# Kernel optimization log

Hardware: AMD Instinct MI355X
Metric: run time of the kernel (lower is better)

## Reference

```python
import jax, jax.numpy as jnp
import numpy as np

B, S, D, L, H = 2, 2048, 2048, 3, 16
DH = D // H
BLOCK = 16
NA = 64
Q = NA * BLOCK
KV = S + Q
VOCAB = 32000
MASK_ID = 31999
GAMMA = 7.0
EPS = 1e-6


def _rope(x, pos):
    # x: [B,H,T,DH], pos: [B,T]
    half = DH // 2
    inv = 1.0 / (10000.0 ** (jnp.arange(half, dtype=jnp.float32) / half))
    ang = pos[:, None, :, None].astype(jnp.float32) * inv  # [B,1,T,half]
    c, s = jnp.cos(ang), jnp.sin(ang)
    x1, x2 = x[..., :half], x[..., half:]
    return jnp.concatenate([x1 * c - x2 * s, x2 * c + x1 * s], axis=-1)


def setup_inputs() -> dict:
    key = jax.random.key(0)
    ks = jax.random.split(key, 12)
    w = lambda k, shp: 0.02 * jax.random.normal(k, shp, jnp.float32)
    return {
        'input_ids': jax.random.randint(ks[0], (B, S), 0, VOCAB, dtype=jnp.int32),
        'hidden_states': jax.random.normal(ks[1], (L, B, S, D), jnp.float32),
        'loss_mask': jnp.ones((B, S), jnp.int32),
        'lm_head_weight': w(ks[2], (VOCAB, D)),
        'norm_weight': jnp.ones((D,), jnp.float32),
        'anchor_positions': jnp.sort(jax.random.randint(ks[3], (B, NA), 0, S - BLOCK, dtype=jnp.int32), axis=-1),
        'ctx_proj_w': w(ks[4], (D, L * D)),
        'embed_table': w(ks[5], (VOCAB, D)),
        'wq': w(ks[6], (D, D)),
        'wk': w(ks[7], (D, D)),
        'wv': w(ks[8], (D, D)),
        'wo': w(ks[9], (D, D)),
    }


def reference(input_ids, hidden_states, loss_mask, lm_head_weight, norm_weight,
              anchor_positions, ctx_proj_w, embed_table, wq, wk, wv, wo):
    # --- context feature: concat L target-layer hiddens, project to D ---
    ctx_cat = jnp.transpose(hidden_states, (1, 2, 0, 3)).reshape(B, S, L * D)
    ctx = jnp.einsum('bsf,df->bsd', ctx_cat, ctx_proj_w)

    # --- position ids (context: 0..S-1; draft block i starts at anchor_i) ---
    ctx_pos = jnp.broadcast_to(jnp.arange(S, dtype=jnp.int32), (B, S))
    draft_pos = (anchor_positions[:, :, None] + jnp.arange(BLOCK, dtype=jnp.int32)[None, None, :]).reshape(B, Q)

    # --- draft input (anchor token + MASKs) and labels ---
    off = jnp.arange(Q, dtype=jnp.int32) % BLOCK                       # [Q]
    anchor_per_tok = jnp.repeat(anchor_positions, BLOCK, axis=1)       # [B,Q]
    anchor_tok = jnp.take_along_axis(input_ids, anchor_positions, axis=1)
    draft_ids = jnp.where(off[None, :] == 0, jnp.repeat(anchor_tok, BLOCK, axis=1), MASK_ID)
    labels = jnp.where(off[None, :] == 0, -100,
                       jnp.take_along_axis(input_ids, anchor_per_tok + off[None, :], axis=1))

    # --- block-causal mask: [B,Q,KV] ---
    qi = jnp.arange(Q, dtype=jnp.int32)
    ki = jnp.arange(KV, dtype=jnp.int32)
    qb = qi // BLOCK                                                   # [Q]
    apos = anchor_positions[:, qb]                                     # [B,Q]
    ctx_vis = (ki[None, None, :] < S) & (ki[None, None, :] < apos[:, :, None])
    kb = (ki - S) // BLOCK
    draft_vis = (ki >= S)[None, :] & (qb[:, None] == kb[None, :])      # [Q,KV]
    mask = ctx_vis | draft_vis[None]                                   # [B,Q,KV]

    # --- single RoPE attention layer: draft queries over [context; draft] ---
    emb = embed_table[draft_ids]                                       # [B,Q,D]
    x_kv = jnp.concatenate([ctx, emb], axis=1)                         # [B,KV,D]
    pos_kv = jnp.concatenate([ctx_pos, draft_pos], axis=1)             # [B,KV]
    q = _rope((emb @ wq.T).reshape(B, Q, H, DH).transpose(0, 2, 1, 3), draft_pos)
    k = _rope((x_kv @ wk.T).reshape(B, KV, H, DH).transpose(0, 2, 1, 3), pos_kv)
    v = (x_kv @ wv.T).reshape(B, KV, H, DH).transpose(0, 2, 1, 3)
    scores = jnp.einsum('bhqd,bhkd->bhqk', q, k) / np.float32(np.sqrt(DH))
    scores = jnp.where(mask[:, None], scores, jnp.float32(-1e30))
    attn = jax.nn.softmax(scores, axis=-1)
    out = jnp.einsum('bhqk,bhkd->bhqd', attn, v).transpose(0, 2, 1, 3).reshape(B, Q, D) @ wo.T
    hidden = emb + out

    # --- RMSNorm + LM head ---
    hidden = hidden * jax.lax.rsqrt(jnp.mean(hidden * hidden, -1, keepdims=True) + EPS) * norm_weight
    logits = hidden @ lm_head_weight.T                                 # [B,Q,VOCAB]

    # --- decay-weighted CE loss + accuracy ---
    logp = jax.nn.log_softmax(logits, axis=-1)
    lab = jnp.where(labels < 0, 0, labels)
    nll = -jnp.take_along_axis(logp, lab[..., None], axis=-1)[..., 0]
    valid = labels != -100
    offf = off.astype(jnp.float32)
    decay = jnp.where(off == 0, 0.0, jnp.exp(-(offf - 1.0) / GAMMA))   # [Q]
    w = decay[None, :] * valid.astype(jnp.float32)
    loss = jnp.sum(nll * w) / jnp.maximum(jnp.sum(w), 1e-6)
    preds = jnp.argmax(logits, axis=-1).astype(labels.dtype)
    acc = jnp.sum((preds == labels) & valid) / jnp.maximum(jnp.sum(valid), 1)
    return loss, acc.astype(jnp.float32)
```

## Files before the change

### kernel.cpp

```cpp
#include <hip/hip_runtime.h>

#define B_ 2
#define S_ 2048
#define D_ 2048
#define L_ 3
#define H_ 16
#define DH_ 128
#define BLK_ 16
#define NA_ 64
#define Q_ 1024
#define KV_ 3072
#define VOCAB_ 32000
#define MASK_ID_ 31999
#define NTOK_ (B_*Q_)
#define VT2_ (VOCAB_/256)
#define NCHUNK_ 4

typedef __attribute__((ext_vector_type(8))) short bf16x8;
typedef __attribute__((ext_vector_type(4))) float f32x4;
typedef const __attribute__((address_space(1))) void* gptr_t;
typedef __attribute__((address_space(3))) void* lptr_t;

__device__ inline unsigned short f2bf(float x) {
  unsigned int u = __float_as_uint(x);
  unsigned int r = (u + 0x7fff + ((u >> 16) & 1)) >> 16;
  return (unsigned short)r;
}
__device__ inline float bf2f(unsigned short u) {
  return __uint_as_float(((unsigned int)u) << 16);
}

__global__ void k_meta(const int* __restrict__ ids, const int* __restrict__ anchors,
                       int* __restrict__ dids, int* __restrict__ dpos, int* __restrict__ labels) {
  int t = blockIdx.x * 256 + threadIdx.x;
  if (t >= NTOK_) return;
  int b = t >> 10, qi = t & 1023;
  int a = qi >> 4, off = qi & 15;
  int ap = anchors[b * NA_ + a];
  dpos[t] = ap + off;
  dids[t] = (off == 0) ? ids[b * S_ + ap] : MASK_ID_;
  labels[t] = (off == 0) ? -100 : ids[b * S_ + ap + off];
}

__global__ void k_cvt(const float* __restrict__ in, unsigned short* __restrict__ out, int n4) {
  int i = blockIdx.x * 256 + threadIdx.x;
  if (i >= n4) return;
  float4 v = ((const float4*)in)[i];
  ushort4 o;
  o.x = f2bf(v.x); o.y = f2bf(v.y); o.z = f2bf(v.z); o.w = f2bf(v.w);
  ((ushort4*)out)[i] = o;
}

__global__ void k_cvt_ctx(const float* __restrict__ hs, unsigned short* __restrict__ out) {
  int bi = blockIdx.x;
  int l = bi % 3, row = bi / 3;
  const float4* src = (const float4*)(hs + ((size_t)l * B_ * S_ + row) * (size_t)D_);
  ushort4* dst = (ushort4*)(out + (size_t)row * (3 * D_) + (size_t)l * D_);
  for (int i = threadIdx.x; i < D_ / 4; i += 256) {
    float4 v = src[i];
    ushort4 o;
    o.x = f2bf(v.x); o.y = f2bf(v.y); o.z = f2bf(v.z); o.w = f2bf(v.w);
    dst[i] = o;
  }
}

__global__ void k_gather(const float* __restrict__ table, const int* __restrict__ dids,
                         unsigned short* __restrict__ x_kv) {
  int row = blockIdx.x;
  int b = row >> 10, qi = row & 1023;
  const float4* src = (const float4*)(table + (size_t)dids[row] * D_);
  ushort4* dst = (ushort4*)(x_kv + ((size_t)b * KV_ + S_ + qi) * D_);
  for (int i = threadIdx.x; i < D_ / 4; i += 256) {
    float4 v = src[i];
    ushort4 o;
    o.x = f2bf(v.x); o.y = f2bf(v.y); o.z = f2bf(v.z); o.w = f2bf(v.w);
    dst[i] = o;
  }
}

#define STAGE2(buf_, kt_)                                                      \
  {                                                                            \
    _Pragma("unroll")                                                          \
    for (int i_ = 0; i_ < 4; ++i_) {                                           \
      __builtin_amdgcn_global_load_lds((gptr_t)(A + aoff[i_] + (kt_)),         \
          (lptr_t)((char*)Asl2 + (buf_) * 32768 + abase[i_]), 16, 0, 0);       \
      __builtin_amdgcn_global_load_lds((gptr_t)(Bw + boff[i_] + (kt_)),        \
          (lptr_t)((char*)Bsl2 + (buf_) * 32768 + bbase[i_]), 16, 0, 0);       \
    }                                                                          \
  }

__global__ __launch_bounds__(512, 1) void k_gemm2(
    const unsigned short* __restrict__ A, const unsigned short* __restrict__ Bw,
    int M, int N, int K,
    const int* __restrict__ labels, float* __restrict__ pm, float* __restrict__ ps,
    int* __restrict__ pbi, float* __restrict__ plab) {
  __shared__ unsigned short Asl2[2 * 256 * 64];
  __shared__ unsigned short Bsl2[2 * 256 * 64];
  int ntm = M >> 8;
  int per = gridDim.x >> 3;
  int wgid = (blockIdx.x & 7) * per + (blockIdx.x >> 3);
  int by = wgid % ntm, bx = wgid / ntm;
  int rowbase = by << 8, colbase = bx << 8;
  int tid = threadIdx.x, l = tid & 63, w = tid >> 6;
  int wm = w >> 2, wn = w & 3;
  int lo = l & 15, hi = l >> 4;

  long long aoff[4], boff[4];
  int abase[4], bbase[4];
#pragma unroll
  for (int i = 0; i < 4; ++i) {
    int rb8 = (w * 4 + i) * 8;
    int r = rb8 + (l >> 3);
    int cu = (l & 7) ^ (r & 7);
    aoff[i] = (long long)(rowbase + r) * K + cu * 8;
    boff[i] = (long long)(colbase + r) * K + cu * 8;
    abase[i] = rb8 * 128;
    bbase[i] = rb8 * 128;
  }
  int ard[8][2], brd[4][2];
#pragma unroll
  for (int m = 0; m < 8; ++m)
#pragma unroll
    for (int ks = 0; ks < 2; ++ks) {
      int r = wm * 128 + m * 16 + lo;
      int p = ((ks << 2) | hi) ^ (r & 7);
      ard[m][ks] = r * 64 + p * 8;
    }
#pragma unroll
  for (int n = 0; n < 4; ++n)
#pragma unroll
    for (int ks = 0; ks < 2; ++ks) {
      int r = wn * 64 + n * 16 + lo;
      int p = ((ks << 2) | hi) ^ (r & 7);
      brd[n][ks] = r * 64 + p * 8;
    }

  f32x4 acc[8][4];
#pragma unroll
  for (int m = 0; m < 8; ++m)
#pragma unroll
    for (int n = 0; n < 4; ++n) acc[m][n] = (f32x4){0.f, 0.f, 0.f, 0.f};

  int NT = K >> 6;
  int cur = 0;
  STAGE2(0, 0);
  for (int t = 0; t < NT; ++t) {
    if (t + 1 < NT) {
      STAGE2(cur ^ 1, (t + 1) << 6);
      asm volatile("s_waitcnt vmcnt(8)" ::: "memory");
    } else {
      asm volatile("s_waitcnt vmcnt(0)" ::: "memory");
    }
    __builtin_amdgcn_s_barrier();
    asm volatile("" ::: "memory");
    const unsigned short* as_ = Asl2 + cur * 16384;
    const unsigned short* bs_ = Bsl2 + cur * 16384;
    __builtin_amdgcn_s_setprio(1);
#pragma unroll
    for (int ks = 0; ks < 2; ++ks) {
      bf16x8 af[8], bg[4];
#pragma unroll
      for (int m = 0; m < 8; ++m) af[m] = *(const bf16x8*)(as_ + ard[m][ks]);
#pragma unroll
      for (int n = 0; n < 4; ++n) bg[n] = *(const bf16x8*)(bs_ + brd[n][ks]);
#pragma unroll
      for (int m = 0; m < 8; ++m)
#pragma unroll
        for (int n = 0; n < 4; ++n)
          acc[m][n] = __builtin_amdgcn_mfma_f32_16x16x32_bf16(af[m], bg[n], acc[m][n], 0, 0, 0);
    }
    __builtin_amdgcn_s_setprio(0);
    __builtin_amdgcn_sched_barrier(0);
    asm volatile("" ::: "memory");
    __builtin_amdgcn_s_barrier();
    cur ^= 1;
  }

  float* f = (float*)Asl2;
  int* ii = (int*)Bsl2;
  __syncthreads();
  if (tid < 256) { f[2304 + tid] = -3.0e38f; ii[1280 + tid] = labels[rowbase + tid]; }
  __syncthreads();
#pragma unroll
  for (int m = 0; m < 8; ++m)
#pragma unroll
    for (int r4 = 0; r4 < 4; ++r4) {
      int rl = wm * 128 + m * 16 + hi * 4 + r4;
      float mx = acc[m][0][r4];
      int arg = colbase + wn * 64 + lo;
#pragma unroll
      for (int n = 1; n < 4; ++n) {
        float v = acc[m][n][r4];
        int c = colbase + wn * 64 + n * 16 + lo;
        if (v > mx) { mx = v; arg = c; }
      }
#pragma unroll
      for (int d = 1; d < 16; d <<= 1) {
        float om = __shfl_xor(mx, d);
        int oc = __shfl_xor(arg, d);
        if (om > mx || (om == mx && oc < arg)) { mx = om; arg = oc; }
      }
      if (lo == 0) { f[wn * 256 + rl] = mx; ii[wn * 256 + rl] = arg; }
    }
  __syncthreads();
  if (tid < 256) {
    float m0 = f[tid]; int a0 = ii[tid];
#pragma unroll
    for (int x = 1; x < 4; ++x) {
      float v = f[x * 256 + tid]; int c = ii[x * 256 + tid];
      if (v > m0 || (v == m0 && c < a0)) { m0 = v; a0 = c; }
    }
    f[2048 + tid] = m0; ii[1024 + tid] = a0;
  }
  __syncthreads();
#pragma unroll
  for (int m = 0; m < 8; ++m)
#pragma unroll
    for (int r4 = 0; r4 < 4; ++r4) {
      int rl = wm * 128 + m * 16 + hi * 4 + r4;
      float gm = f[2048 + rl];
      float sacc = 0.f;
#pragma unroll
      for (int n = 0; n < 4; ++n) sacc += __expf(acc[m][n][r4] - gm);
#pragma unroll
      for (int d = 1; d < 16; d <<= 1) sacc += __shfl_xor(sacc, d);
      if (lo == 0) f[1024 + wn * 256 + rl] = sacc;
      int lab = ii[1280 + rl];
      int rel = lab - colbase;
      if (rel >= 0 && rel < 256 && (rel >> 6) == wn && (rel & 15) == lo) {
        int n_own = (rel >> 4) & 3;
#pragma unroll
        for (int n = 0; n < 4; ++n)
          if (n == n_own) f[2304 + rl] = acc[m][n][r4];
      }
    }
  __syncthreads();
  if (tid < 256) {
    int grow = rowbase + tid;
    size_t p = (size_t)grow * VT2_ + bx;
    pm[p] = f[2048 + tid];
    ps[p] = f[1024 + tid] + f[1024 + 256 + tid] + f[1024 + 512 + tid] + f[1024 + 768 + tid];
    pbi[p] = ii[1024 + tid];
    plab[p] = f[2304 + tid];
  }
}

template <int CMODE>
__global__ __launch_bounds__(256) void k_mfma_bt(
    const unsigned short* __restrict__ A, const unsigned short* __restrict__ Bw,
    float* __restrict__ Cf, unsigned short* __restrict__ Cb,
    int M, int N, int K, int adivlog, long long abump, int cdivlog, long long cbump) {
  __shared__ unsigned short As[128 * 32];
  __shared__ unsigned short Bs[128 * 32];
  int ntn = N >> 7;
  int bx = blockIdx.x % ntn, by = blockIdx.x / ntn;
  int rowbase = by << 7, colbase = bx << 7;
  int tid = threadIdx.x, lane = tid & 63, w = tid >> 6;
  int wr = w >> 1, wc = w & 1;
  int lo = lane & 15, hi = lane >> 4;

  f32x4 acc[4][4];
#pragma unroll
  for (int m = 0; m < 4; ++m)
#pragma unroll
    for (int n = 0; n < 4; ++n) acc[m][n] = (f32x4){0.f, 0.f, 0.f, 0.f};

  for (int kt = 0; kt < K; kt += 32) {
#pragma unroll
    for (int i = 0; i < 2; ++i) {
      int seg = i * 4 + w;
      int rloc = seg * 16 + (lane >> 2);
      int kcol = kt + ((lane & 3) << 3);
      int ra = rowbase + rloc;
      long long aoff = (long long)ra * K + (long long)(ra >> adivlog) * abump + kcol;
      __builtin_amdgcn_global_load_lds((gptr_t)(A + aoff), (lptr_t)(As + seg * 512), 16, 0, 0);
      int rb = colbase + rloc;
      long long boff = (long long)rb * K + kcol;
      __builtin_amdgcn_global_load_lds((gptr_t)(Bw + boff), (lptr_t)(Bs + seg * 512), 16, 0, 0);
    }
    __syncthreads();
    bf16x8 af[4], bfv[4];
#pragma unroll
    for (int m = 0; m < 4; ++m) {
      int row = wr * 64 + m * 16 + lo;
      af[m] = *(const bf16x8*)(As + row * 32 + (hi << 3));
    }
#pragma unroll
    for (int n = 0; n < 4; ++n) {
      int row = wc * 64 + n * 16 + lo;
      bfv[n] = *(const bf16x8*)(Bs + row * 32 + (hi << 3));
    }
#pragma unroll
    for (int m = 0; m < 4; ++m)
#pragma unroll
      for (int n = 0; n < 4; ++n)
        acc[m][n] = __builtin_amdgcn_mfma_f32_16x16x32_bf16(af[m], bfv[n], acc[m][n], 0, 0, 0);
    __syncthreads();
  }

  if (CMODE == 0 || CMODE == 1) {
#pragma unroll
    for (int m = 0; m < 4; ++m)
#pragma unroll
      for (int n = 0; n < 4; ++n)
#pragma unroll
        for (int r4 = 0; r4 < 4; ++r4) {
          int row = rowbase + wr * 64 + m * 16 + hi * 4 + r4;
          int col = colbase + wc * 64 + n * 16 + lo;
          size_t addr = (size_t)row * N + (size_t)(row >> cdivlog) * cbump + col;
          if (CMODE == 0) Cf[addr] = acc[m][n][r4];
          else Cb[addr] = f2bf(acc[m][n][r4]);
        }
  } else {
#pragma unroll
    for (int m = 0; m < 4; ++m)
#pragma unroll
      for (int n = 0; n < 4; ++n)
#pragma unroll
        for (int r4 = 0; r4 < 4; ++r4) {
          int row = rowbase + wr * 64 + m * 16 + hi * 4 + r4;
          int col = colbase + wc * 64 + n * 16 + lo;
          int bb = row >= KV_;
          int kv = row - bb * KV_;
          size_t addr = ((size_t)(bb * H_ + (col >> 7)) * 128 + (col & 127)) * KV_ + kv;
          Cb[addr] = f2bf(acc[m][n][r4]);
        }
  }
}

__global__ void k_rope(unsigned short* __restrict__ x, const int* __restrict__ dpos, int mode) {
  int idx = blockIdx.x * 256 + threadIdx.x;
  int j = idx & 63;
  int h = (idx >> 6) & 15;
  int row = idx >> 10;
  int pos;
  if (mode == 0) {
    if (row >= NTOK_) return;
    pos = dpos[row];
  } else {
    if (row >= B_ * KV_) return;
    int b = row / KV_, kvi = row % KV_;
    pos = (kvi < S_) ? kvi : dpos[b * Q_ + (kvi - S_)];
  }
  float inv = expf(-(float)j * (9.210340371976184f / 64.f));
  float ang = (float)pos * inv;
  float c = cosf(ang), s = sinf(ang);
  unsigned short* p = x + (size_t)row * D_ + h * DH_ + j;
  float x1 = bf2f(p[0]), x2 = bf2f(p[64]);
  p[0] = f2bf(x1 * c - x2 * s);
  p[64] = f2bf(x2 * c + x1 * s);
}

__global__ __launch_bounds__(256) void k_attn_part(
    const unsigned short* __restrict__ qb, const unsigned short* __restrict__ kb,
    const unsigned short* __restrict__ vt, const int* __restrict__ anchors,
    float* __restrict__ pm_att, float* __restrict__ pl_att, float* __restrict__ po_att) {
  __shared__ __align__(16) unsigned short P_all[4][16 * 40];
  int w = threadIdx.x >> 6, lane = threadIdx.x & 63;
  int blk = blockIdx.x * 4 + w;
  int chunk = blk & 3, h = (blk >> 2) & 15, a = (blk >> 6) & 63, b = blk >> 12;
  int ql = lane & 15, p = lane >> 4;
  int apos = anchors[b * NA_ + a];

  int cstart = chunk << 9;
  int cend = min(apos, cstart + 512);
  int len = (cend > cstart) ? (cend - cstart) : 0;
  int ntile = (len + 31) >> 5;
  int total = ntile + ((chunk == 3) ? 1 : 0);

  if (total == 0) {
    if (p == 0) { pm_att[blk * 16 + ql] = -3.0e38f; pl_att[blk * 16 + ql] = 0.f; }
    return;
  }
  unsigned short* P = P_all[w];

  const unsigned short* qbase = qb + ((size_t)(b * Q_ + a * 16 + ql)) * D_ + h * DH_;
  bf16x8 qf[4];
#pragma unroll
  for (int ks = 0; ks < 4; ++ks)
    qf[ks] = *(const bf16x8*)(qbase + ks * 32 + p * 8);

  const unsigned short* kbb = kb + (size_t)b * KV_ * D_ + h * DH_;
  const unsigned short* vtb = vt + ((size_t)(b * H_ + h)) * 128 * KV_;

  f32x4 o[8];
#pragma unroll
  for (int nt = 0; nt < 8; ++nt) o[nt] = (f32x4){0.f, 0.f, 0.f, 0.f};
  float mrun = -3.0e38f, lrun = 0.f;
  const float scl = 0.08838834764831845f;

  for (int t = 0; t < total; ++t) {
    bool isdraft = (chunk == 3) && (t == ntile);
    int ktb = isdraft ? (S_ + a * 16) : (cstart + (t << 5));
    int vc = isdraft ? 16 : min(32, cend - ktb);
    float s[2][4];
#pragma unroll
    for (int g = 0; g < 2; ++g) {
      if (g * 16 < vc) {
        f32x4 accs = (f32x4){0.f, 0.f, 0.f, 0.f};
        const unsigned short* krow = kbb + (size_t)(ktb + g * 16 + ql) * D_;
#pragma unroll
        for (int ks = 0; ks < 4; ++ks) {
          bf16x8 kf = *(const bf16x8*)(krow + ks * 32 + p * 8);
          accs = __builtin_amdgcn_mfma_f32_16x16x32_bf16(kf, qf[ks], accs, 0, 0, 0);
        }
#pragma unroll
        for (int r = 0; r < 4; ++r) {
          int kl = g * 16 + p * 4 + r;
          s[g][r] = (kl < vc) ? accs[r] * scl : -3.0e38f;
        }
      } else {
#pragma unroll
        for (int r = 0; r < 4; ++r) s[g][r] = -3.0e38f;
      }
    }
    float mt = s[0][0];
#pragma unroll
    for (int g = 0; g < 2; ++g)
#pragma unroll
      for (int r = 0; r < 4; ++r) mt = fmaxf(mt, s[g][r]);
    mt = fmaxf(mt, __shfl_xor(mt, 16));
    mt = fmaxf(mt, __shfl_xor(mt, 32));
    float mnew = fmaxf(mrun, mt);
    float corr = __expf(mrun - mnew);
    float psum = 0.f;
#pragma unroll
    for (int g = 0; g < 2; ++g) {
      float p0 = __expf(s[g][0] - mnew), p1 = __expf(s[g][1] - mnew);
      float p2 = __expf(s[g][2] - mnew), p3 = __expf(s[g][3] - mnew);
      psum += p0 + p1 + p2 + p3;
      ushort2 w0, w1;
      w0.x = f2bf(p0); w0.y = f2bf(p1); w1.x = f2bf(p2); w1.y = f2bf(p3);
      int eo = ql * 40 + g * 16 + p * 4;
      *(ushort2*)(P + eo) = w0;
      *(ushort2*)(P + eo + 2) = w1;
    }
    psum += __shfl_xor(psum, 16);
    psum += __shfl_xor(psum, 32);
    lrun = lrun * corr + psum;
    mrun = mnew;
    float cr[4];
#pragma unroll
    for (int r = 0; r < 4; ++r) cr[r] = __shfl(corr, p * 4 + r);
#pragma unroll
    for (int nt = 0; nt < 8; ++nt)
#pragma unroll
      for (int r = 0; r < 4; ++r) o[nt][r] *= cr[r];
    bf16x8 pf = *(const bf16x8*)(P + ql * 40 + p * 8);
#pragma unroll
    for (int nt = 0; nt < 8; ++nt) {
      bf16x8 vf = *(const bf16x8*)(vtb + (size_t)(nt * 16 + ql) * KV_ + ktb + p * 8);
      o[nt] = __builtin_amdgcn_mfma_f32_16x16x32_bf16(pf, vf, o[nt], 0, 0, 0);
    }
  }
  if (p == 0) { pm_att[blk * 16 + ql] = mrun; pl_att[blk * 16 + ql] = lrun; }
  float* pob = po_att + (size_t)blk * 2048;
#pragma unroll
  for (int nt = 0; nt < 8; ++nt)
#pragma unroll
    for (int r = 0; r < 4; ++r)
      pob[(p * 4 + r) * 128 + nt * 16 + ql] = o[nt][r];
}

__global__ __launch_bounds__(256) void k_attn_combine(
    const float* __restrict__ pm_att, const float* __restrict__ pl_att,
    const float* __restrict__ po_att, unsigned short* __restrict__ ob) {
  int base = blockIdx.x;
  int h = base & 15, a = (base >> 4) & 63, b = base >> 10;
  int d = threadIdx.x & 127, qh = threadIdx.x >> 7;
  int pbase = base * 4;
#pragma unroll
  for (int qq = 0; qq < 8; ++qq) {
    int q = qh * 8 + qq;
    float m0 = pm_att[(pbase + 0) * 16 + q], m1 = pm_att[(pbase + 1) * 16 + q];
    float m2 = pm_att[(pbase + 2) * 16 + q], m3 = pm_att[(pbase + 3) * 16 + q];
    float mg = fmaxf(fmaxf(m0, m1), fmaxf(m2, m3));
    float w0 = __expf(m0 - mg), w1 = __expf(m1 - mg);
    float w2 = __expf(m2 - mg), w3 = __expf(m3 - mg);
    float lg = pl_att[(pbase + 0) * 16 + q] * w0 + pl_att[(pbase + 1) * 16 + q] * w1 +
               pl_att[(pbase + 2) * 16 + q] * w2 + pl_att[(pbase + 3) * 16 + q] * w3;
    float od = po_att[(size_t)(pbase + 0) * 2048 + q * 128 + d] * w0 +
               po_att[(size_t)(pbase + 1) * 2048 + q * 128 + d] * w1 +
               po_att[(size_t)(pbase + 2) * 2048 + q * 128 + d] * w2 +
               po_att[(size_t)(pbase + 3) * 2048 + q * 128 + d] * w3;
    ob[((size_t)(b * Q_ + a * 16 + q)) * D_ + h * DH_ + d] = f2bf(od / lg);
  }
}

__global__ void k_rmsnorm(const unsigned short* __restrict__ x_kv, const float* __restrict__ proj,
                          const float* __restrict__ nw, unsigned short* __restrict__ outp) {
  int row = blockIdx.x;
  int b = row >> 10, qi = row & 1023;
  const unsigned short* emb = x_kv + ((size_t)b * KV_ + S_ + qi) * D_;
  const float* pr = proj + (size_t)row * D_;
  __shared__ float red[256];
  float h[8];
  float ssum = 0.f;
#pragma unroll
  for (int i = 0; i < 8; ++i) {
    int d = threadIdx.x + i * 256;
    h[i] = bf2f(emb[d]) + pr[d];
    ssum += h[i] * h[i];
  }
  red[threadIdx.x] = ssum;
  __syncthreads();
  for (int s = 128; s; s >>= 1) {
    if (threadIdx.x < s) red[threadIdx.x] += red[threadIdx.x + s];
    __syncthreads();
  }
  float scale = rsqrtf(red[0] / (float)D_ + 1e-6f);
#pragma unroll
  for (int i = 0; i < 8; ++i) {
    int d = threadIdx.x + i * 256;
    outp[(size_t)row * D_ + d] = f2bf(h[i] * scale * nw[d]);
  }
}

__global__ void k_combine(const float* __restrict__ pm, const float* __restrict__ ps,
                          const int* __restrict__ pbi, const float* __restrict__ plab,
                          const int* __restrict__ labels, float* __restrict__ ts) {
  int t = blockIdx.x * 256 + threadIdx.x;
  if (t >= NTOK_) return;
  const float* pmr = pm + (size_t)t * VT2_;
  const float* psr = ps + (size_t)t * VT2_;
  const int* pbir = pbi + (size_t)t * VT2_;
  const float* plabr = plab + (size_t)t * VT2_;
  float M = -3.0e38f; int bi = 0;
  for (int x = 0; x < VT2_; ++x) {
    float v = pmr[x];
    if (v > M) { M = v; bi = pbir[x]; }
  }
  float ssum = 0.f, labl = -3.0e38f;
  for (int x = 0; x < VT2_; ++x) {
    ssum += psr[x] * __expf(pmr[x] - M);
    labl = fmaxf(labl, plabr[x]);
  }
  float lse = M + logf(ssum);
  int lab = labels[t];
  int off = t & 15;
  float valid = (lab != -100) ? 1.f : 0.f;
  float w = (off == 0) ? 0.f : __expf(-(float)(off - 1) / 7.0f);
  w *= valid;
  float nll = (lab != -100) ? (lse - labl) : 0.f;
  float correct = (valid > 0.f && bi == lab) ? 1.f : 0.f;
  ts[t * 4 + 0] = nll * w;
  ts[t * 4 + 1] = w;
  ts[t * 4 + 2] = correct;
  ts[t * 4 + 3] = valid;
}

__global__ void k_finalize(const float* __restrict__ ts, float* __restrict__ out) {
  __shared__ float r0[256], r1[256], r2[256], r3[256];
  int tid = threadIdx.x;
  float s0 = 0, s1 = 0, s2 = 0, s3 = 0;
  for (int t = tid; t < NTOK_; t += 256) {
    s0 += ts[t * 4 + 0]; s1 += ts[t * 4 + 1];
    s2 += ts[t * 4 + 2]; s3 += ts[t * 4 + 3];
  }
  r0[tid] = s0; r1[tid] = s1; r2[tid] = s2; r3[tid] = s3;
  __syncthreads();
  for (int s = 128; s; s >>= 1) {
    if (tid < s) {
      r0[tid] += r0[tid + s]; r1[tid] += r1[tid + s];
      r2[tid] += r2[tid + s]; r3[tid] += r3[tid + s];
    }
    __syncthreads();
  }
  if (tid == 0) {
    out[0] = r0[0] / fmaxf(r1[0], 1e-6f);
    out[1] = r2[0] / fmaxf(r3[0], 1.f);
  }
}

extern "C" void kernel_launch(void* const* d_in, const int* in_sizes, int n_in,
                              void* d_out, int out_size, void* d_ws, size_t ws_size,
                              hipStream_t stream) {
  const int* input_ids = (const int*)d_in[0];
  const float* hs = (const float*)d_in[1];
  const float* lm_head = (const float*)d_in[3];
  const float* norm_w = (const float*)d_in[4];
  const int* anchors = (const int*)d_in[5];
  const float* ctx_w = (const float*)d_in[6];
  const float* embed = (const float*)d_in[7];
  const float* wq = (const float*)d_in[8];
  const float* wk = (const float*)d_in[9];
  const float* wv = (const float*)d_in[10];
  const float* wo = (const float*)d_in[11];
  float* out = (float*)d_out;

  char* base = (char*)d_ws;
  size_t off = 0;
  unsigned short* x_kv_bf = (unsigned short*)(base + off); off += (size_t)B_ * KV_ * D_ * 2;
  unsigned short* wkb = (unsigned short*)(base + off); off += (size_t)D_ * D_ * 2;
  unsigned short* wvb = (unsigned short*)(base + off); off += (size_t)D_ * D_ * 2;
  unsigned short* wqb = (unsigned short*)(base + off); off += (size_t)D_ * D_ * 2;
  unsigned short* wob = (unsigned short*)(base + off); off += (size_t)D_ * D_ * 2;
  unsigned short* hidden_bf = (unsigned short*)(base + off); off += (size_t)NTOK_ * D_ * 2;
  unsigned short* attn_bf = (unsigned short*)(base + off); off += (size_t)NTOK_ * D_ * 2;
  float* proj = (float*)(base + off); off += (size_t)NTOK_ * D_ * 4;
  float* pm = (float*)(base + off); off += (size_t)NTOK_ * VT2_ * 4;
  float* psum = (float*)(base + off); off += (size_t)NTOK_ * VT2_ * 4;
  float* plab = (float*)(base + off); off += (size_t)NTOK_ * VT2_ * 4;
  int* pbi = (int*)(base + off); off += (size_t)NTOK_ * VT2_ * 4;
  float* tstats = (float*)(base + off); off += (size_t)NTOK_ * 4 * 4;
  int* dids = (int*)(base + off); off += NTOK_ * 4;
  int* dpos = (int*)(base + off); off += NTOK_ * 4;
  int* labels = (int*)(base + off); off += NTOK_ * 4;
  char* regA = base + off;
  const size_t SLACK = 65536;
  unsigned short* ctxA = (unsigned short*)(regA);
  unsigned short* ctx_wbf = (unsigned short*)(regA + 50331648);
  unsigned short* kbuf = (unsigned short*)(regA + 50331648 + 25165824);
  unsigned short* vtbuf = (unsigned short*)(regA + 50331648 + 2 * 25165824 + SLACK);
  unsigned short* qbuf = (unsigned short*)(regA + 50331648 + 3 * 25165824 + 2 * SLACK);
  unsigned short* lm_bf = (unsigned short*)(regA);
  float* po_att = (float*)(regA);
  float* pm_att = (float*)(regA + 67108864);
  float* pl_att = (float*)(regA + 67108864 + 524288);

  k_meta<<<(NTOK_ + 255) / 256, 256, 0, stream>>>(input_ids, anchors, dids, dpos, labels);
  k_cvt<<<((D_ * (L_ * D_) / 4) + 255) / 256, 256, 0, stream>>>(ctx_w, ctx_wbf, D_ * (L_ * D_) / 4);
  k_cvt<<<((D_ * D_ / 4) + 255) / 256, 256, 0, stream>>>(wk, wkb, D_ * D_ / 4);
  k_cvt<<<((D_ * D_ / 4) + 255) / 256, 256, 0, stream>>>(wv, wvb, D_ * D_ / 4);
  k_cvt<<<((D_ * D_ / 4) + 255) / 256, 256, 0, stream>>>(wq, wqb, D_ * D_ / 4);
  k_cvt<<<((D_ * D_ / 4) + 255) / 256, 256, 0, stream>>>(wo, wob, D_ * D_ / 4);
  k_cvt_ctx<<<B_ * S_ * L_, 256, 0, stream>>>(hs, ctxA);
  k_gather<<<NTOK_, 256, 0, stream>>>(embed, dids, x_kv_bf);

  k_mfma_bt<1><<<(4096 / 128) * (2048 / 128), 256, 0, stream>>>(
      ctxA, ctx_wbf, nullptr, x_kv_bf, 4096, 2048, 6144, 30, 0LL, 11, (long long)Q_ * D_);
  k_mfma_bt<1><<<(6144 / 128) * (2048 / 128), 256, 0, stream>>>(
      x_kv_bf, wkb, nullptr, kbuf, 6144, 2048, 2048, 30, 0LL, 30, 0LL);
  k_mfma_bt<3><<<(6144 / 128) * (2048 / 128), 256, 0, stream>>>(
      x_kv_bf, wvb, nullptr, vtbuf, 6144, 2048, 2048, 30, 0LL, 30, 0LL);
  k_mfma_bt<1><<<(2048 / 128) * (2048 / 128), 256, 0, stream>>>(
      x_kv_bf + (size_t)S_ * D_, wqb, nullptr, qbuf, 2048, 2048, 2048, 10,
      (long long)(KV_ - Q_) * D_, 30, 0LL);
  k_rope<<<(NTOK_ * H_ * 64) / 256, 256, 0, stream>>>(qbuf, dpos, 0);
  k_rope<<<(B_ * KV_ * H_ * 64) / 256, 256, 0, stream>>>(kbuf, dpos, 1);
  k_attn_part<<<(B_ * NA_ * H_ * NCHUNK_) / 4, 256, 0, stream>>>(
      qbuf, kbuf, vtbuf, anchors, pm_att, pl_att, po_att);
  k_attn_combine<<<B_ * NA_ * H_, 256, 0, stream>>>(pm_att, pl_att, po_att, attn_bf);
  k_mfma_bt<0><<<(2048 / 128) * (2048 / 128), 256, 0, stream>>>(
      attn_bf, wob, proj, nullptr, 2048, 2048, 2048, 30, 0LL, 30, 0LL);
  k_rmsnorm<<<NTOK_, 256, 0, stream>>>(x_kv_bf, proj, norm_w, hidden_bf);
  k_cvt<<<((VOCAB_ * D_ / 4) + 255) / 256, 256, 0, stream>>>(lm_head, lm_bf, VOCAB_ * D_ / 4);
  k_gemm2<<<(2048 / 256) * (VOCAB_ / 256), 512, 0, stream>>>(
      hidden_bf, lm_bf, 2048, VOCAB_, 2048, labels, pm, psum, pbi, plab);
  k_combine<<<(NTOK_ + 255) / 256, 256, 0, stream>>>(pm, psum, pbi, plab, labels, tstats);
  k_finalize<<<1, 256, 0, stream>>>(tstats, out);
}
```

Before: 1.211 ms.

## Add double-buffered 128x256 direct-to-LDS GEMM for context and K projections

Adds a new 512-thread GEMM kernel with 128x256 tiles and a K-step of 64. Tiles are loaded straight into LDS with global_load_lds, using XOR-swizzled layouts and two buffers so the next tile loads while the current one is computed. Blocks are remapped across XCD-sized groups to improve L2 locality. The kernel replaces the 128x128 generic GEMM for the context projection and the K projection, aiming for more reuse per tile and better overlap of memory and compute, at the cost of larger LDS use and one workgroup per CU.

```diff
diff --git a/kernel.cpp b/kernel.cpp
--- a/kernel.cpp
+++ b/kernel.cpp
@@ -243,6 +243,123 @@
     pbi[p] = ii[1024 + tid];
     plab[p] = f[2304 + tid];
   }
+}
+
+#define STAGE2B(buf_, kt_)                                                     \
+  {                                                                            \
+    _Pragma("unroll")                                                          \
+    for (int i_ = 0; i_ < 2; ++i_)                                             \
+      __builtin_amdgcn_global_load_lds((gptr_t)(A + aoff[i_] + (kt_)),         \
+          (lptr_t)((char*)Asl + (buf_) * 16384 + abase[i_]), 16, 0, 0);        \
+    _Pragma("unroll")                                                          \
+    for (int i_ = 0; i_ < 4; ++i_)                                             \
+      __builtin_amdgcn_global_load_lds((gptr_t)(Bw + boff[i_] + (kt_)),        \
+          (lptr_t)((char*)Bsl + (buf_) * 32768 + bbase[i_]), 16, 0, 0);        \
+  }
+
+__global__ __launch_bounds__(512, 1) void k_gemm2b(
+    const unsigned short* __restrict__ A, const unsigned short* __restrict__ Bw,
+    unsigned short* __restrict__ Cb,
+    int M, int N, int K, int cdivlog, long long cbump) {
+  __shared__ unsigned short Asl[2 * 128 * 64];
+  __shared__ unsigned short Bsl[2 * 256 * 64];
+  int ntm = M >> 7;
+  int per = gridDim.x >> 3;
+  int wgid = (blockIdx.x & 7) * per + (blockIdx.x >> 3);
+  int by = wgid % ntm, bx = wgid / ntm;
+  int rowbase = by << 7, colbase = bx << 8;
+  int tid = threadIdx.x, l = tid & 63, w = tid >> 6;
+  int wm = w >> 2, wn = w & 3;
+  int lo = l & 15, hi = l >> 4;
+
+  long long aoff[2]; int abase[2];
+#pragma unroll
+  for (int i = 0; i < 2; ++i) {
+    int rb8 = i * 64 + w * 8;
+    int r = rb8 + (l >> 3);
+    int cu = (l & 7) ^ (r & 7);
+    aoff[i] = (long long)(rowbase + r) * K + cu * 8;
+    abase[i] = rb8 * 128;
+  }
+  long long boff[4]; int bbase[4];
+#pragma unroll
+  for (int i = 0; i < 4; ++i) {
+    int rb8 = (w * 4 + i) * 8;
+    int r = rb8 + (l >> 3);
+    int cu = (l & 7) ^ (r & 7);
+    boff[i] = (long long)(colbase + r) * K + cu * 8;
+    bbase[i] = rb8 * 128;
+  }
+  int ard[4][2], brd[4][2];
+#pragma unroll
+  for (int m = 0; m < 4; ++m)
+#pragma unroll
+    for (int ks = 0; ks < 2; ++ks) {
+      int r = wm * 64 + m * 16 + lo;
+      int p = ((ks << 2) | hi) ^ (r & 7);
+      ard[m][ks] = r * 64 + p * 8;
+    }
+#pragma unroll
+  for (int n = 0; n < 4; ++n)
+#pragma unroll
+    for (int ks = 0; ks < 2; ++ks) {
+      int r = wn * 64 + n * 16 + lo;
+      int p = ((ks << 2) | hi) ^ (r & 7);
+      brd[n][ks] = r * 64 + p * 8;
+    }
+
+  f32x4 acc[4][4];
+#pragma unroll
+  for (int m = 0; m < 4; ++m)
+#pragma unroll
+    for (int n = 0; n < 4; ++n) acc[m][n] = (f32x4){0.f, 0.f, 0.f, 0.f};
+
+  int NT = K >> 6;
+  int cur = 0;
+  STAGE2B(0, 0);
+  for (int t = 0; t < NT; ++t) {
+    if (t + 1 < NT) {
+      STAGE2B(cur ^ 1, (t + 1) << 6);
+      asm volatile("s_waitcnt vmcnt(6)" ::: "memory");
+    } else {
+      asm volatile("s_waitcnt vmcnt(0)" ::: "memory");
+    }
+    __builtin_amdgcn_s_barrier();
+    asm volatile("" ::: "memory");
+    const unsigned short* as_ = Asl + cur * 8192;
+    const unsigned short* bs_ = Bsl + cur * 16384;
+    __builtin_amdgcn_s_setprio(1);
+#pragma unroll
+    for (int ks = 0; ks < 2; ++ks) {
+      bf16x8 af[4], bg[4];
+#pragma unroll
+      for (int m = 0; m < 4; ++m) af[m] = *(const bf16x8*)(as_ + ard[m][ks]);
+#pragma unroll
+      for (int n = 0; n < 4; ++n) bg[n] = *(const bf16x8*)(bs_ + brd[n][ks]);
+#pragma unroll
+      for (int m = 0; m < 4; ++m)
+#pragma unroll
+        for (int n = 0; n < 4; ++n)
+          acc[m][n] = __builtin_amdgcn_mfma_f32_16x16x32_bf16(af[m], bg[n], acc[m][n], 0, 0, 0);
+    }
+    __builtin_amdgcn_s_setprio(0);
+    __builtin_amdgcn_sched_barrier(0);
+    asm volatile("" ::: "memory");
+    __builtin_amdgcn_s_barrier();
+    cur ^= 1;
+  }
+
+#pragma unroll
+  for (int m = 0; m < 4; ++m)
+#pragma unroll
+    for (int n = 0; n < 4; ++n)
+#pragma unroll
+      for (int r4 = 0; r4 < 4; ++r4) {
+        int row = rowbase + wm * 64 + m * 16 + hi * 4 + r4;
+        int col = colbase + wn * 64 + n * 16 + lo;
+        size_t addr = (size_t)row * N + (size_t)(row >> cdivlog) * cbump + col;
+        Cb[addr] = f2bf(acc[m][n][r4]);
+      }
 }
 
 template <int CMODE>
@@ -627,10 +744,10 @@
   k_cvt_ctx<<<B_ * S_ * L_, 256, 0, stream>>>(hs, ctxA);
   k_gather<<<NTOK_, 256, 0, stream>>>(embed, dids, x_kv_bf);
 
-  k_mfma_bt<1><<<(4096 / 128) * (2048 / 128), 256, 0, stream>>>(
-      ctxA, ctx_wbf, nullptr, x_kv_bf, 4096, 2048, 6144, 30, 0LL, 11, (long long)Q_ * D_);
-  k_mfma_bt<1><<<(6144 / 128) * (2048 / 128), 256, 0, stream>>>(
-      x_kv_bf, wkb, nullptr, kbuf, 6144, 2048, 2048, 30, 0LL, 30, 0LL);
+  k_gemm2b<<<(4096 / 128) * (2048 / 256), 512, 0, stream>>>(
+      ctxA, ctx_wbf, x_kv_bf, 4096, 2048, 6144, 11, (long long)Q_ * D_);
+  k_gemm2b<<<(6144 / 128) * (2048 / 256), 512, 0, stream>>>(
+      x_kv_bf, wkb, kbuf, 6144, 2048, 2048, 30, 0LL);
   k_mfma_bt<3><<<(6144 / 128) * (2048 / 128), 256, 0, stream>>>(
       x_kv_bf, wvb, nullptr, vtbuf, 6144, 2048, 2048, 30, 0LL, 30, 0LL);
   k_mfma_bt<1><<<(2048 / 128) * (2048 / 128), 256, 0, stream>>>(
```

Measured after the change: 1.258 ms. +3.8%, slower.

## Fuse K and V projections into one 256x256-tile GEMM with split epilogue

Applied to the files above, without the earlier changes.

Concatenates the bf16 K and V weights into one contiguous buffer and computes both projections in a single launch of the larger 256x256-tile pipelined GEMM (k_gemm2). A templated epilogue writes row-major K for columns below D and transposed V for the rest. The aim is to read the shared activation operand once, cut a launch, and use the faster double-buffered kernel in place of the 128-tile one. The new weight buffer is placed in the overlapping scratch region, which could alias other buffers, and the V epilogue does strided transposed stores.

```diff
diff --git a/kernel.cpp b/kernel.cpp
--- a/kernel.cpp
+++ b/kernel.cpp
@@ -89,8 +89,10 @@
     }                                                                          \
   }
 
+template <int CMODE>
 __global__ __launch_bounds__(512, 1) void k_gemm2(
     const unsigned short* __restrict__ A, const unsigned short* __restrict__ Bw,
+    unsigned short* __restrict__ Ck, unsigned short* __restrict__ Cvt,
     int M, int N, int K,
     const int* __restrict__ labels, float* __restrict__ pm, float* __restrict__ ps,
     int* __restrict__ pbi, float* __restrict__ plab) {
@@ -176,6 +178,36 @@
     cur ^= 1;
   }
 
+  if (CMODE == 4) {
+    if (colbase < D_) {
+#pragma unroll
+      for (int m = 0; m < 8; ++m)
+#pragma unroll
+        for (int n = 0; n < 4; ++n)
+#pragma unroll
+          for (int r4 = 0; r4 < 4; ++r4) {
+            int row = rowbase + wm * 128 + m * 16 + hi * 4 + r4;
+            int col = colbase + wn * 64 + n * 16 + lo;
+            Ck[(size_t)row * D_ + col] = f2bf(acc[m][n][r4]);
+          }
+    } else {
+#pragma unroll
+      for (int m = 0; m < 8; ++m)
+#pragma unroll
+        for (int n = 0; n < 4; ++n)
+#pragma unroll
+          for (int r4 = 0; r4 < 4; ++r4) {
+            int row = rowbase + wm * 128 + m * 16 + hi * 4 + r4;
+            int c2 = colbase - D_ + wn * 64 + n * 16 + lo;
+            int bb = row >= KV_;
+            int kv = row - bb * KV_;
+            size_t addr = ((size_t)(bb * H_ + (c2 >> 7)) * 128 + (c2 & 127)) * KV_ + kv;
+            Cvt[addr] = f2bf(acc[m][n][r4]);
+          }
+    }
+    return;
+  }
+
   float* f = (float*)Asl2;
   int* ii = (int*)Bsl2;
   __syncthreads();
@@ -298,34 +330,18 @@
     __syncthreads();
   }
 
-  if (CMODE == 0 || CMODE == 1) {
-#pragma unroll
-    for (int m = 0; m < 4; ++m)
-#pragma unroll
-      for (int n = 0; n < 4; ++n)
-#pragma unroll
-        for (int r4 = 0; r4 < 4; ++r4) {
-          int row = rowbase + wr * 64 + m * 16 + hi * 4 + r4;
-          int col = colbase + wc * 64 + n * 16 + lo;
-          size_t addr = (size_t)row * N + (size_t)(row >> cdivlog) * cbump + col;
-          if (CMODE == 0) Cf[addr] = acc[m][n][r4];
-          else Cb[addr] = f2bf(acc[m][n][r4]);
-        }
-  } else {
-#pragma unroll
-    for (int m = 0; m < 4; ++m)
-#pragma unroll
-      for (int n = 0; n < 4; ++n)
-#pragma unroll
-        for (int r4 = 0; r4 < 4; ++r4) {
-          int row = rowbase + wr * 64 + m * 16 + hi * 4 + r4;
-          int col = colbase + wc * 64 + n * 16 + lo;
-          int bb = row >= KV_;
-          int kv = row - bb * KV_;
-          size_t addr = ((size_t)(bb * H_ + (col >> 7)) * 128 + (col & 127)) * KV_ + kv;
-          Cb[addr] = f2bf(acc[m][n][r4]);
-        }
-  }
+#pragma unroll
+  for (int m = 0; m < 4; ++m)
+#pragma unroll
+    for (int n = 0; n < 4; ++n)
+#pragma unroll
+      for (int r4 = 0; r4 < 4; ++r4) {
+        int row = rowbase + wr * 64 + m * 16 + hi * 4 + r4;
+        int col = colbase + wc * 64 + n * 16 + lo;
+        size_t addr = (size_t)row * N + (size_t)(row >> cdivlog) * cbump + col;
+        if (CMODE == 0) Cf[addr] = acc[m][n][r4];
+        else Cb[addr] = f2bf(acc[m][n][r4]);
+      }
 }
 
 __global__ void k_rope(unsigned short* __restrict__ x, const int* __restrict__ dpos, int mode) {
@@ -591,8 +607,6 @@
   char* base = (char*)d_ws;
   size_t off = 0;
   unsigned short* x_kv_bf = (unsigned short*)(base + off); off += (size_t)B_ * KV_ * D_ * 2;
-  unsigned short* wkb = (unsigned short*)(base + off); off += (size_t)D_ * D_ * 2;
-  unsigned short* wvb = (unsigned short*)(base + off); off += (size_t)D_ * D_ * 2;
   unsigned short* wqb = (unsigned short*)(base + off); off += (size_t)D_ * D_ * 2;
   unsigned short* wob = (unsigned short*)(base + off); off += (size_t)D_ * D_ * 2;
   unsigned short* hidden_bf = (unsigned short*)(base + off); off += (size_t)NTOK_ * D_ * 2;
@@ -613,6 +627,7 @@
   unsigned short* kbuf = (unsigned short*)(regA + 50331648 + 25165824);
   unsigned short* vtbuf = (unsigned short*)(regA + 50331648 + 2 * 25165824 + SLACK);
   unsigned short* qbuf = (unsigned short*)(regA + 50331648 + 3 * 25165824 + 2 * SLACK);
+  unsigned short* wkvb = (unsigned short*)(regA + 50331648 + 3 * 25165824 + 2 * SLACK + 8388608);
   unsigned short* lm_bf = (unsigned short*)(regA);
   float* po_att = (float*)(regA);
   float* pm_att = (float*)(regA + 67108864);
@@ -620,8 +635,8 @@
 
   k_meta<<<(NTOK_ + 255) / 256, 256, 0, stream>>>(input_ids, anchors, dids, dpos, labels);
   k_cvt<<<((D_ * (L_ * D_) / 4) + 255) / 256, 256, 0, stream>>>(ctx_w, ctx_wbf, D_ * (L_ * D_) / 4);
-  k_cvt<<<((D_ * D_ / 4) + 255) / 256, 256, 0, stream>>>(wk, wkb, D_ * D_ / 4);
-  k_cvt<<<((D_ * D_ / 4) + 255) / 256, 256, 0, stream>>>(wv, wvb, D_ * D_ / 4);
+  k_cvt<<<((D_ * D_ / 4) + 255) / 256, 256, 0, stream>>>(wk, wkvb, D_ * D_ / 4);
+  k_cvt<<<((D_ * D_ / 4) + 255) / 256, 256, 0, stream>>>(wv, wkvb + (size_t)D_ * D_, D_ * D_ / 4);
   k_cvt<<<((D_ * D_ / 4) + 255) / 256, 256, 0, stream>>>(wq, wqb, D_ * D_ / 4);
   k_cvt<<<((D_ * D_ / 4) + 255) / 256, 256, 0, stream>>>(wo, wob, D_ * D_ / 4);
   k_cvt_ctx<<<B_ * S_ * L_, 256, 0, stream>>>(hs, ctxA);
@@ -629,10 +644,9 @@
 
   k_mfma_bt<1><<<(4096 / 128) * (2048 / 128), 256, 0, stream>>>(
       ctxA, ctx_wbf, nullptr, x_kv_bf, 4096, 2048, 6144, 30, 0LL, 11, (long long)Q_ * D_);
-  k_mfma_bt<1><<<(6144 / 128) * (2048 / 128), 256, 0, stream>>>(
-      x_kv_bf, wkb, nullptr, kbuf, 6144, 2048, 2048, 30, 0LL, 30, 0LL);
-  k_mfma_bt<3><<<(6144 / 128) * (2048 / 128), 256, 0, stream>>>(
-      x_kv_bf, wvb, nullptr, vtbuf, 6144, 2048, 2048, 30, 0LL, 30, 0LL);
+  k_gemm2<4><<<(6144 / 256) * (4096 / 256), 512, 0, stream>>>(
+      x_kv_bf, wkvb, kbuf, vtbuf, 6144, 4096, 2048,
+      nullptr, nullptr, nullptr, nullptr, nullptr);
   k_mfma_bt<1><<<(2048 / 128) * (2048 / 128), 256, 0, stream>>>(
       x_kv_bf + (size_t)S_ * D_, wqb, nullptr, qbuf, 2048, 2048, 2048, 10,
       (long long)(KV_ - Q_) * D_, 30, 0LL);
@@ -645,8 +659,9 @@
       attn_bf, wob, proj, nullptr, 2048, 2048, 2048, 30, 0LL, 30, 0LL);
   k_rmsnorm<<<NTOK_, 256, 0, stream>>>(x_kv_bf, proj, norm_w, hidden_bf);
   k_cvt<<<((VOCAB_ * D_ / 4) + 255) / 256, 256, 0, stream>>>(lm_head, lm_bf, VOCAB_ * D_ / 4);
-  k_gemm2<<<(2048 / 256) * (VOCAB_ / 256), 512, 0, stream>>>(
-      hidden_bf, lm_bf, 2048, VOCAB_, 2048, labels, pm, psum, pbi, plab);
+  k_gemm2<2><<<(2048 / 256) * (VOCAB_ / 256), 512, 0, stream>>>(
+      hidden_bf, lm_bf, nullptr, nullptr, 2048, VOCAB_, 2048,
+      labels, pm, psum, pbi, plab);
   k_combine<<<(NTOK_ + 255) / 256, 256, 0, stream>>>(pm, psum, pbi, plab, labels, tstats);
   k_finalize<<<1, 256, 0, stream>>>(tstats, out);
 }
```

New measurement: 1.252 ms. 3.4% more time.

## Split attention context into eight chunks and store partial outputs in bf16

Applied to the files above, without the earlier changes.

Doubles the number of split-KV chunks in the anchor-block attention from 4 to 8, so each wave handles up to 256 context keys instead of 512. This shortens the longest per-wave serial loop and improves load balance. Partial outputs are now written as bf16 rather than fp32, which halves the partial-output traffic. The combine kernel is generalized to loop over NCHUNK_ partials. The costs are a bf16 rounding of unnormalized partial sums, twice as many partials to combine, and relocated pm/pl buffers. The attention launch grid is not visible and must be scaled to match.

```diff
diff --git a/kernel.cpp b/kernel.cpp
--- a/kernel.cpp
+++ b/kernel.cpp
@@ -14,7 +14,7 @@
 #define MASK_ID_ 31999
 #define NTOK_ (B_*Q_)
 #define VT2_ (VOCAB_/256)
-#define NCHUNK_ 4
+#define NCHUNK_ 8
 
 typedef __attribute__((ext_vector_type(8))) short bf16x8;
 typedef __attribute__((ext_vector_type(4))) float f32x4;
@@ -354,19 +354,20 @@
 __global__ __launch_bounds__(256) void k_attn_part(
     const unsigned short* __restrict__ qb, const unsigned short* __restrict__ kb,
     const unsigned short* __restrict__ vt, const int* __restrict__ anchors,
-    float* __restrict__ pm_att, float* __restrict__ pl_att, float* __restrict__ po_att) {
+    float* __restrict__ pm_att, float* __restrict__ pl_att,
+    unsigned short* __restrict__ po_att) {
   __shared__ __align__(16) unsigned short P_all[4][16 * 40];
   int w = threadIdx.x >> 6, lane = threadIdx.x & 63;
   int blk = blockIdx.x * 4 + w;
-  int chunk = blk & 3, h = (blk >> 2) & 15, a = (blk >> 6) & 63, b = blk >> 12;
+  int chunk = blk & 7, h = (blk >> 3) & 15, a = (blk >> 7) & 63, b = blk >> 13;
   int ql = lane & 15, p = lane >> 4;
   int apos = anchors[b * NA_ + a];
 
-  int cstart = chunk << 9;
-  int cend = min(apos, cstart + 512);
+  int cstart = chunk << 8;
+  int cend = min(apos, cstart + 256);
   int len = (cend > cstart) ? (cend - cstart) : 0;
   int ntile = (len + 31) >> 5;
-  int total = ntile + ((chunk == 3) ? 1 : 0);
+  int total = ntile + ((chunk == 7) ? 1 : 0);
 
   if (total == 0) {
     if (p == 0) { pm_att[blk * 16 + ql] = -3.0e38f; pl_att[blk * 16 + ql] = 0.f; }
@@ -390,7 +391,7 @@
   const float scl = 0.08838834764831845f;
 
   for (int t = 0; t < total; ++t) {
-    bool isdraft = (chunk == 3) && (t == ntile);
+    bool isdraft = (chunk == 7) && (t == ntile);
     int ktb = isdraft ? (S_ + a * 16) : (cstart + (t << 5));
     int vc = isdraft ? 16 : min(32, cend - ktb);
     float s[2][4];
@@ -454,35 +455,38 @@
     }
   }
   if (p == 0) { pm_att[blk * 16 + ql] = mrun; pl_att[blk * 16 + ql] = lrun; }
-  float* pob = po_att + (size_t)blk * 2048;
+  unsigned short* pob = po_att + (size_t)blk * 2048;
 #pragma unroll
   for (int nt = 0; nt < 8; ++nt)
 #pragma unroll
     for (int r = 0; r < 4; ++r)
-      pob[(p * 4 + r) * 128 + nt * 16 + ql] = o[nt][r];
+      pob[(p * 4 + r) * 128 + nt * 16 + ql] = f2bf(o[nt][r]);
 }
 
 __global__ __launch_bounds__(256) void k_attn_combine(
     const float* __restrict__ pm_att, const float* __restrict__ pl_att,
-    const float* __restrict__ po_att, unsigned short* __restrict__ ob) {
+    const unsigned short* __restrict__ po_att, unsigned short* __restrict__ ob) {
   int base = blockIdx.x;
   int h = base & 15, a = (base >> 4) & 63, b = base >> 10;
   int d = threadIdx.x & 127, qh = threadIdx.x >> 7;
-  int pbase = base * 4;
+  int pbase = base * NCHUNK_;
 #pragma unroll
   for (int qq = 0; qq < 8; ++qq) {
     int q = qh * 8 + qq;
-    float m0 = pm_att[(pbase + 0) * 16 + q], m1 = pm_att[(pbase + 1) * 16 + q];
-    float m2 = pm_att[(pbase + 2) * 16 + q], m3 = pm_att[(pbase + 3) * 16 + q];
-    float mg = fmaxf(fmaxf(m0, m1), fmaxf(m2, m3));
-    float w0 = __expf(m0 - mg), w1 = __expf(m1 - mg);
-    float w2 = __expf(m2 - mg), w3 = __expf(m3 - mg);
-    float lg = pl_att[(pbase + 0) * 16 + q] * w0 + pl_att[(pbase + 1) * 16 + q] * w1 +
-               pl_att[(pbase + 2) * 16 + q] * w2 + pl_att[(pbase + 3) * 16 + q] * w3;
-    float od = po_att[(size_t)(pbase + 0) * 2048 + q * 128 + d] * w0 +
-               po_att[(size_t)(pbase + 1) * 2048 + q * 128 + d] * w1 +
-               po_att[(size_t)(pbase + 2) * 2048 + q * 128 + d] * w2 +
-               po_att[(size_t)(pbase + 3) * 2048 + q * 128 + d] * w3;
+    float mv[NCHUNK_];
+    float mg = -3.0e38f;
+#pragma unroll
+    for (int c = 0; c < NCHUNK_; ++c) {
+      mv[c] = pm_att[(pbase + c) * 16 + q];
+      mg = fmaxf(mg, mv[c]);
+    }
+    float lg = 0.f, od = 0.f;
+#pragma unroll
+    for (int c = 0; c < NCHUNK_; ++c) {
+      float wc = __expf(mv[c] - mg);
+      lg += pl_att[(pbase + c) * 16 + q] * wc;
+      od += bf2f(po_att[(size_t)(pbase + c) * 2048 + q * 128 + d]) * wc;
+    }
     ob[((size_t)(b * Q_ + a * 16 + q)) * D_ + h * DH_ + d] = f2bf(od / lg);
   }
 }
@@ -614,9 +618,9 @@
   unsigned short* vtbuf = (unsigned short*)(regA + 50331648 + 2 * 25165824 + SLACK);
   unsigned short* qbuf = (unsigned short*)(regA + 50331648 + 3 * 25165824 + 2 * SLACK);
   unsigned short* lm_bf = (unsigned short*)(regA);
-  float* po_att = (float*)(regA);
+  unsigned short* po_att = (unsigned short*)(regA);
   float* pm_att = (float*)(regA + 67108864);
-  float* pl_att = (float*)(regA + 67108864 + 524288);
+  float* pl_att = (float*)(regA + 67108864 + 1048576);
 
   k_meta<<<(NTOK_ + 255) / 256, 256, 0, stream>>>(input_ids, anchors, dids, dpos, labels);
   k_cvt<<<((D_ * (L_ * D_) / 4) + 255) / 256, 256, 0, stream>>>(ctx_w, ctx_wbf, D_ * (L_ * D_) / 4);
```

Measured after the change: 1.267 ms. +4.6%, slower.
